# Kernel optimization log

Hardware: AMD Instinct MI355X
Metric: run time of the kernel (lower is better)

Reference implementation:

```python
import jax, jax.numpy as jnp
import numpy as np

B, S, H = 4, 4096, 768
NB = 16            # n_blocks (first factor)
BSZ = H // NB      # 48, block size
LN_EPS = 1e-12


def setup_inputs() -> dict:
    key = jax.random.key(0)
    ks = jax.random.split(key, 6)
    hidden_states = jax.random.normal(ks[0], (B, S, H), dtype=jnp.float32)
    # Monarch factors: B1 has NB blocks of (BSZ,BSZ); B2 has BSZ blocks of (NB,NB)
    w1_blocks = jax.random.normal(ks[1], (NB, BSZ, BSZ), dtype=jnp.float32) / np.sqrt(BSZ)
    w2_blocks = jax.random.normal(ks[2], (BSZ, NB, NB), dtype=jnp.float32) / np.sqrt(NB)
    gate_w = jax.random.normal(ks[3], (H, H), dtype=jnp.float32) / np.sqrt(H)
    gate_b = jnp.zeros((H,), dtype=jnp.float32)
    out_w = jax.random.normal(ks[4], (H, H), dtype=jnp.float32) / np.sqrt(H)
    out_b = jnp.zeros((H,), dtype=jnp.float32)
    ln_gamma = jnp.ones((H,), dtype=jnp.float32)
    ln_beta = jnp.zeros((H,), dtype=jnp.float32)
    return {
        "hidden_states": hidden_states,
        "w1_blocks": w1_blocks,
        "w2_blocks": w2_blocks,
        "gate_w": gate_w,
        "gate_b": gate_b,
        "out_w": out_w,
        "out_b": out_b,
        "ln_gamma": ln_gamma,
        "ln_beta": ln_beta,
    }


def _monarch(x, w1, w2):
    # x: [B, S, H]; Monarch product P B2 P B1 applied to last dim.
    b, s, h = x.shape
    y = x.reshape(b, s, NB, BSZ)
    y = jnp.einsum('bski,kij->bskj', y, w1)      # block-diag (NB blocks of BSZxBSZ)
    y = jnp.swapaxes(y, -1, -2)                  # permute: [B,S,BSZ,NB]
    y = jnp.einsum('bsqi,qij->bsqj', y, w2)      # block-diag (BSZ blocks of NBxNB)
    y = jnp.swapaxes(y, -1, -2)                  # permute back: [B,S,NB,BSZ]
    return y.reshape(b, s, h)


def _layernorm(x, gamma, beta, eps):
    mu = jnp.mean(x, axis=-1, keepdims=True)
    var = jnp.mean(jnp.square(x - mu), axis=-1, keepdims=True)
    return (x - mu) * jax.lax.rsqrt(var + eps) * gamma + beta


def reference(hidden_states, w1_blocks, w2_blocks, gate_w, gate_b,
              out_w, out_b, ln_gamma, ln_beta):
    residual = hidden_states
    mixed = _monarch(hidden_states, w1_blocks, w2_blocks)
    gate = jax.nn.sigmoid(hidden_states @ gate_w.T + gate_b)
    h = mixed * gate
    h = h @ out_w.T + out_b
    # dropout is identity in eval / p=0
    return _layernorm(h + residual, ln_gamma, ln_beta, LN_EPS)
```

## Files before the change

### kernel.cpp

```cpp
#include <hip/hip_runtime.h>
#include <hip/hip_bf16.h>
#include <stdint.h>

#define HD 768

typedef __attribute__((ext_vector_type(8))) short bf16x8;
typedef __attribute__((ext_vector_type(4))) float f32x4;
typedef __attribute__((ext_vector_type(4))) unsigned short u16x4;

typedef __attribute__((address_space(3))) void lds_void_t;
typedef const __attribute__((address_space(1))) void gbl_void_t;

__device__ inline void gload_lds16(const void* g, void* l) {
  __builtin_amdgcn_global_load_lds((gbl_void_t*)g, (lds_void_t*)l, 16, 0, 0);
}

__device__ inline unsigned short f2bf(float f) {
  union { float f; unsigned int u; } v; v.f = f;
  return (unsigned short)((v.u + 0x7fffu + ((v.u >> 16) & 1u)) >> 16);
}
__device__ inline float bf2f(unsigned short u) {
  union { unsigned int uu; float f; } v; v.uu = ((unsigned int)u) << 16;
  return v.f;
}

#define BAR() asm volatile("s_barrier" ::: "memory")
#define LGKM(N) { asm volatile("s_waitcnt lgkmcnt(" #N ")" ::: "memory"); __builtin_amdgcn_sched_barrier(0); }
#define VMC(N) asm volatile("s_waitcnt vmcnt(" #N ")" ::: "memory")

__global__ void prep_all_kernel(const float* __restrict__ x,
                                const float* __restrict__ gw, const float* __restrict__ ow,
                                const float* __restrict__ w1, const float* __restrict__ w2,
                                unsigned short* __restrict__ xb,
                                unsigned short* __restrict__ Gwb,
                                unsigned short* __restrict__ Opk,
                                unsigned short* __restrict__ w1f,
                                unsigned short* __restrict__ w2f) {
  int bid = blockIdx.x;
  if (bid < 12288) {
    int i = bid * 256 + threadIdx.x;
    float4 v = ((const float4*)x)[i];
    ushort4 o;
    o.x = f2bf(v.x); o.y = f2bf(v.y); o.z = f2bf(v.z); o.w = f2bf(v.w);
    ((ushort4*)xb)[i] = o;
  } else if (bid < 14592) {
    int e = (bid - 12288) * 256 + threadIdx.x;
    Gwb[e] = f2bf(gw[e]);
  } else if (bid < 14880) {
    int r = (bid - 14592) * 256 + threadIdx.x;
    int lane = r & 63;
    int ks = (r >> 6) % 24;
    int nt = r / (24 * 64);
    int n = nt * 16 + (lane & 15);
    int k = ks * 32 + (lane >> 4) * 8;
    bf16x8 pack;
#pragma unroll
    for (int j = 0; j < 8; ++j) pack[j] = (short)f2bf(ow[(size_t)n * HD + k + j]);
    *(bf16x8*)(Opk + (size_t)r * 8) = pack;
  } else if (bid < 14904) {
    int e = (bid - 14880) * 256 + threadIdx.x;
    int lane = e & 63, fi = e >> 6;
    int ks = fi & 1, nt = (fi >> 1) % 3, k = fi / 6;
    int lrr = lane & 15, lgg = lane >> 4;
    int q = nt * 16 + lrr;
    bf16x8 pack;
#pragma unroll
    for (int j = 0; j < 8; ++j) {
      int kk = ks * 32 + lgg * 8 + j;
      float v = (kk < 48) ? w1[(k * 48 + kk) * 48 + q] : 0.0f;
      pack[j] = (short)f2bf(v);
    }
    *(bf16x8*)(w1f + (size_t)e * 8) = pack;
  } else {
    int e = (bid - 14904) * 256 + threadIdx.x;
    int lane = e & 63, q = e >> 6;
    int lrr = lane & 15, lgg = lane >> 4;
    bf16x8 pack;
#pragma unroll
    for (int j = 0; j < 8; ++j) {
      int kk = lgg * 8 + j;
      float v = (kk < 16) ? w2[(q * 16 + kk) * 16 + lrr] : 0.0f;
      pack[j] = (short)f2bf(v);
    }
    *(bf16x8*)(w2f + (size_t)e * 8) = pack;
  }
}

__global__ __launch_bounds__(256, 2)
void monarch_kernel(const unsigned short* __restrict__ xb,
                    const unsigned short* __restrict__ w1f,
                    const unsigned short* __restrict__ w2f,
                    unsigned short* __restrict__ mx) {
  __shared__ __align__(16) unsigned char zl[49152];
  const int tid = threadIdx.x, lane = tid & 63, wid = tid >> 6;
  const int lr = lane & 15, lg = lane >> 4;
  const size_t m0 = (size_t)blockIdx.x * 32;

#pragma unroll
  for (int kb = 0; kb < 4; ++kb) {
    const int k = wid * 4 + kb;
    const unsigned short* wf = w1f + (size_t)(k * 6) * 512 + lane * 8;
    bf16x8 b00 = *(const bf16x8*)(wf + 0 * 512);
    bf16x8 b01 = *(const bf16x8*)(wf + 1 * 512);
    bf16x8 b10 = *(const bf16x8*)(wf + 2 * 512);
    bf16x8 b11 = *(const bf16x8*)(wf + 3 * 512);
    bf16x8 b20 = *(const bf16x8*)(wf + 4 * 512);
    bf16x8 b21 = *(const bf16x8*)(wf + 5 * 512);
#pragma unroll
    for (int mt = 0; mt < 2; ++mt) {
      const unsigned short* ar = xb + (m0 + mt * 16 + lr) * 768 + k * 48;
      bf16x8 a0 = *(const bf16x8*)(ar + lg * 8);
      bf16x8 a1 = (bf16x8){0, 0, 0, 0, 0, 0, 0, 0};
      if (lg < 2) a1 = *(const bf16x8*)(ar + 32 + lg * 8);
      f32x4 c0 = {0, 0, 0, 0}, c1 = {0, 0, 0, 0}, c2 = {0, 0, 0, 0};
      c0 = __builtin_amdgcn_mfma_f32_16x16x32_bf16(a0, b00, c0, 0, 0, 0);
      c0 = __builtin_amdgcn_mfma_f32_16x16x32_bf16(a1, b01, c0, 0, 0, 0);
      c1 = __builtin_amdgcn_mfma_f32_16x16x32_bf16(a0, b10, c1, 0, 0, 0);
      c1 = __builtin_amdgcn_mfma_f32_16x16x32_bf16(a1, b11, c1, 0, 0, 0);
      c2 = __builtin_amdgcn_mfma_f32_16x16x32_bf16(a0, b20, c2, 0, 0, 0);
      c2 = __builtin_amdgcn_mfma_f32_16x16x32_bf16(a1, b21, c2, 0, 0, 0);
#pragma unroll
      for (int i = 0; i < 4; ++i) {
        int row = mt * 16 + lg * 4 + i;
        int base = row * 1536 + k * 2;
        int swz = (row & 7) << 4;
        *(unsigned short*)(zl + ((base + (0 * 16 + lr) * 32) ^ swz)) = f2bf(c0[i]);
        *(unsigned short*)(zl + ((base + (1 * 16 + lr) * 32) ^ swz)) = f2bf(c1[i]);
        *(unsigned short*)(zl + ((base + (2 * 16 + lr) * 32) ^ swz)) = f2bf(c2[i]);
      }
    }
  }
  __syncthreads();

  unsigned int upk[2][4][6];
#pragma unroll
  for (int qq = 0; qq < 12; ++qq) {
    const int q = wid * 12 + qq;
    bf16x8 bw = *(const bf16x8*)(w2f + (size_t)q * 512 + lane * 8);
#pragma unroll
    for (int mt = 0; mt < 2; ++mt) {
      int row = mt * 16 + lr;
      int off = (row * 1536 + (lg < 2 ? q * 32 + lg * 16 : 0)) ^ ((row & 7) << 4);
      bf16x8 a = *(const bf16x8*)(zl + off);
      if (lg >= 2) a = (bf16x8){0, 0, 0, 0, 0, 0, 0, 0};
      f32x4 c = {0, 0, 0, 0};
      c = __builtin_amdgcn_mfma_f32_16x16x32_bf16(a, bw, c, 0, 0, 0);
#pragma unroll
      for (int i = 0; i < 4; ++i) {
        unsigned int h = (unsigned int)f2bf(c[i]);
        if (qq & 1) upk[mt][i][qq >> 1] |= (h << 16);
        else        upk[mt][i][qq >> 1] = h;
      }
    }
  }
  __syncthreads();

  const int wq0 = wid * 12;
#pragma unroll
  for (int mt = 0; mt < 2; ++mt) {
#pragma unroll
    for (int i = 0; i < 4; ++i) {
      int row = mt * 16 + lg * 4 + i;
      int base = row * 1536 + lr * 96 + wq0 * 2;
      int swz = (row & 7) << 4;
#pragma unroll
      for (int p = 0; p < 3; ++p) {
        uint2 v; v.x = upk[mt][i][p * 2]; v.y = upk[mt][i][p * 2 + 1];
        *(uint2*)(zl + ((base + p * 8) ^ swz)) = v;
      }
    }
  }
  __syncthreads();

#pragma unroll
  for (int p = 0; p < 12; ++p) {
    int id = p * 256 + tid;
    int row = id / 96, w16 = id % 96;
    int by = (row * 1536 + w16 * 16) ^ ((row & 7) << 4);
    f32x4 v = *(const f32x4*)(zl + by);
    *(f32x4*)((unsigned char*)mx + (m0 + row) * 1536 + w16 * 16) = v;
  }
}

__global__ __launch_bounds__(256, 2)
void gate_mix_kernel(const unsigned short* __restrict__ xb,
                     const unsigned short* __restrict__ Gwb,
                     const float* __restrict__ gate_b,
                     const unsigned short* __restrict__ mx,
                     unsigned short* __restrict__ hb) {
  __shared__ __align__(16) unsigned char lds[81920];
  const int tid = threadIdx.x, lane = tid & 63;
  const int wid = tid >> 6, wm = wid >> 1, wn = wid & 1;
  const int lr = lane & 15, lg = lane >> 4;

  const int b = blockIdx.x;
  const int work = (b & 7) * 64 + (b >> 3);
  const int panel = work >> 2, nwin = work & 3;
  const size_t m0 = (size_t)panel * 128;
  const int n0 = nwin * 192;

  const int r0 = tid >> 3;
  const int sw = ((tid & 7) << 4) ^ ((r0 & 7) << 4);
  const int o0 = (0 * 32 + r0) * 1536 + sw;
  const int o1 = (1 * 32 + r0) * 1536 + sw;
  const int o2 = (2 * 32 + r0) * 1536 + sw;
  const int o3 = (3 * 32 + r0) * 1536 + sw;
  const int o4 = (4 * 32 + r0) * 1536 + sw;
  const int o5 = (5 * 32 + r0) * 1536 + sw;
  const unsigned char* aS = (const unsigned char*)xb + m0 * 1536;
  const unsigned char* bS = (const unsigned char*)Gwb + (size_t)n0 * 1536;

#define STAGE_A(KT, BUF) { const unsigned char* sp = aS + (KT) * 128; \
    gload_lds16(sp + o0, lds + (BUF) * 16384 + tid * 16); \
    gload_lds16(sp + o1, lds + (BUF) * 16384 + 4096 + tid * 16); \
    gload_lds16(sp + o2, lds + (BUF) * 16384 + 8192 + tid * 16); \
    gload_lds16(sp + o3, lds + (BUF) * 16384 + 12288 + tid * 16); }
#define STAGE_B(KT, BUF) { const unsigned char* sp = bS + (KT) * 128; \
    gload_lds16(sp + o0, lds + 32768 + (BUF) * 24576 + tid * 16); \
    gload_lds16(sp + o1, lds + 32768 + (BUF) * 24576 + 4096 + tid * 16); \
    gload_lds16(sp + o2, lds + 32768 + (BUF) * 24576 + 8192 + tid * 16); \
    gload_lds16(sp + o3, lds + 32768 + (BUF) * 24576 + 12288 + tid * 16); \
    gload_lds16(sp + o4, lds + 32768 + (BUF) * 24576 + 16384 + tid * 16); \
    gload_lds16(sp + o5, lds + 32768 + (BUF) * 24576 + 20480 + tid * 16); }

  const int sx0 = (lg * 16) ^ ((lr & 7) << 4);
  const int sx1 = sx0 ^ 64;
  const unsigned char* baA0 = lds + (wm * 64 + lr) * 128 + sx0;
  const unsigned char* baA1 = lds + (wm * 64 + lr) * 128 + sx1;
  const unsigned char* baB0 = lds + 32768 + (wn * 96 + lr) * 128 + sx0;
  const unsigned char* baB1 = lds + 32768 + (wn * 96 + lr) * 128 + sx1;

  f32x4 acc[4][6];
#pragma unroll
  for (int mt = 0; mt < 4; ++mt)
#pragma unroll
    for (int nt = 0; nt < 6; ++nt) acc[mt][nt] = (f32x4){0, 0, 0, 0};

  bf16x8 aA[4], aB[4];
  bf16x8 bB0[6], bB1[6];

#define RD_AA(BUF) { _Pragma("unroll") for (int mt = 0; mt < 4; ++mt) \
      aA[mt] = *(const bf16x8*)(baA0 + (BUF) * 16384 + mt * 2048); }
#define RD_AB(BUF) { _Pragma("unroll") for (int mt = 0; mt < 4; ++mt) \
      aB[mt] = *(const bf16x8*)(baA1 + (BUF) * 16384 + mt * 2048); }
#define RD_B0(BUF) { _Pragma("unroll") for (int nt = 0; nt < 6; ++nt) \
      bB0[nt] = *(const bf16x8*)(baB0 + (BUF) * 24576 + nt * 2048); }
#define RD_B1(BUF) { _Pragma("unroll") for (int nt = 0; nt < 6; ++nt) \
      bB1[nt] = *(const bf16x8*)(baB1 + (BUF) * 24576 + nt * 2048); }
#define MM24(AR, BR) { __builtin_amdgcn_s_setprio(1); \
    _Pragma("unroll") for (int mt = 0; mt < 4; ++mt) \
    _Pragma("unroll") for (int nt = 0; nt < 6; ++nt) \
      acc[mt][nt] = __builtin_amdgcn_mfma_f32_16x16x32_bf16(AR[mt], BR[nt], acc[mt][nt], 0, 0, 0); \
    __builtin_amdgcn_s_setprio(0); }

#define KT_BODY(KT, BUF, STG, VN) { \
    RD_AB(BUF); RD_B1(BUF); \
    LGKM(10); MM24(aA, bB0); \
    LGKM(0); \
    BAR(); \
    if (STG) { STAGE_A((KT) + 2, BUF); STAGE_B((KT) + 2, BUF); } \
    VMC(VN); \
    BAR(); \
    RD_AA((BUF) ^ 1); RD_B0((BUF) ^ 1); \
    MM24(aB, bB1); }

  STAGE_A(0, 0); STAGE_B(0, 0); STAGE_A(1, 1); STAGE_B(1, 1);
  VMC(10);
  BAR();
  RD_AA(0); RD_B0(0);

#pragma unroll 1
  for (int kt = 0; kt < 10; kt += 2) {
    KT_BODY(kt, 0, 1, 10);
    KT_BODY(kt + 1, 1, 1, 10);
  }
  KT_BODY(10, 0, 0, 0);
  RD_AB(1); RD_B1(1);
  LGKM(10); MM24(aA, bB0);
  LGKM(0);  MM24(aB, bB1);

#pragma unroll
  for (int nt = 0; nt < 6; ++nt) {
    const int col = n0 + wn * 96 + nt * 16 + lr;
    const float gbv = gate_b[col];
#pragma unroll
    for (int mt = 0; mt < 4; ++mt) {
#pragma unroll
      for (int i = 0; i < 4; ++i) {
        size_t row = m0 + wm * 64 + mt * 16 + lg * 4 + i;
        float g = acc[mt][nt][i] + gbv;
        float s = 1.0f / (1.0f + __expf(-g));
        float mval = bf2f(mx[row * 768 + col]);
        hb[row * 768 + col] = f2bf(s * mval);
      }
    }
  }
#undef STAGE_A
#undef STAGE_B
#undef RD_AA
#undef RD_AB
#undef RD_B0
#undef RD_B1
#undef MM24
#undef KT_BODY
}

__global__ __launch_bounds__(512, 2)
void out_ln_kernel(const unsigned short* __restrict__ hb,
                   const unsigned short* __restrict__ Opk,
                   const float* __restrict__ out_b,
                   const unsigned short* __restrict__ xb,
                   const float* __restrict__ gamma,
                   const float* __restrict__ beta,
                   float* __restrict__ out) {
  __shared__ __align__(16) unsigned char lds[16384];
  __shared__ float psum[64][8];
  __shared__ float psq[64][8];

  const int tid = threadIdx.x, lane = tid & 63, wid = tid >> 6;
  const int lr = lane & 15, lg = lane >> 4;
  const size_t m0 = (size_t)blockIdx.x * 64;

  const int srow = tid >> 3;
  const unsigned char* aSrc = (const unsigned char*)hb + (m0 + srow) * 1536
                              + (((tid & 7) << 4) ^ ((srow & 7) << 4));
#define STAGE_A(KT, BUF) gload_lds16(aSrc + (KT) * 128, lds + (BUF) * 8192 + tid * 16)

  const unsigned short* bBase = Opk + ((size_t)(wid * 6) * 24 * 64 + lane) * 8;
#define LOAD_B(KT, BR) { _Pragma("unroll") for (int nt = 0; nt < 6; ++nt) { \
      BR[nt * 2 + 0] = *(const bf16x8*)(bBase + nt * 12288 + ((KT) * 2 + 0) * 512); \
      BR[nt * 2 + 1] = *(const bf16x8*)(bBase + nt * 12288 + ((KT) * 2 + 1) * 512); } }

  const int sx0 = (lg * 16) ^ ((lr & 7) << 4);
  const unsigned char* baA0 = lds + lr * 128 + sx0;
  const unsigned char* baA1 = lds + lr * 128 + (sx0 ^ 64);
#define RD_A(BUF) { _Pragma("unroll") for (int mt = 0; mt < 4; ++mt) { \
      aF0[mt] = *(const bf16x8*)(baA0 + (BUF) * 8192 + mt * 2048); \
      aF1[mt] = *(const bf16x8*)(baA1 + (BUF) * 8192 + mt * 2048); } }

#define MM48(BR) { __builtin_amdgcn_s_setprio(1); \
    _Pragma("unroll") for (int mt = 0; mt < 4; ++mt) \
    _Pragma("unroll") for (int nt = 0; nt < 6; ++nt) { \
      acc[mt][nt] = __builtin_amdgcn_mfma_f32_16x16x32_bf16(aF0[mt], BR[nt * 2 + 0], acc[mt][nt], 0, 0, 0); \
      acc[mt][nt] = __builtin_amdgcn_mfma_f32_16x16x32_bf16(aF1[mt], BR[nt * 2 + 1], acc[mt][nt], 0, 0, 0); } \
    __builtin_amdgcn_s_setprio(0); }

  f32x4 acc[4][6];
#pragma unroll
  for (int mt = 0; mt < 4; ++mt)
#pragma unroll
    for (int nt = 0; nt < 6; ++nt) acc[mt][nt] = (f32x4){0, 0, 0, 0};

  bf16x8 aF0[4], aF1[4];
  bf16x8 bP[12], bQ[12];

#define KT_BODY(KT, BUF, BCUR, BNXT, LAST) { \
    if (!(LAST)) { STAGE_A((KT) + 1, (BUF) ^ 1); LOAD_B((KT) + 1, BNXT); } \
    RD_A(BUF); \
    LGKM(0); \
    if (!(LAST)) { VMC(13); } else { VMC(0); } \
    MM48(BCUR); \
    if (!(LAST)) { VMC(12); BAR(); } }

  STAGE_A(0, 0);
  LOAD_B(0, bP);
  VMC(12);
  BAR();

#pragma unroll 1
  for (int kt = 0; kt < 10; kt += 2) {
    KT_BODY(kt, 0, bP, bQ, 0);
    KT_BODY(kt + 1, 1, bQ, bP, 0);
  }
  KT_BODY(10, 0, bP, bQ, 0);
  KT_BODY(11, 1, bQ, bP, 1);

#pragma unroll
  for (int nt = 0; nt < 6; ++nt) {
    const int col = wid * 96 + nt * 16 + lr;
    const float obv = out_b[col];
#pragma unroll
    for (int mt = 0; mt < 4; ++mt) {
#pragma unroll
      for (int i = 0; i < 4; ++i) {
        size_t row = m0 + mt * 16 + lg * 4 + i;
        acc[mt][nt][i] += obv + bf2f(xb[row * 768 + col]);
      }
    }
  }
#pragma unroll
  for (int mt = 0; mt < 4; ++mt) {
#pragma unroll
    for (int i = 0; i < 4; ++i) {
      float s = 0.f, q = 0.f;
#pragma unroll
      for (int nt = 0; nt < 6; ++nt) { float v = acc[mt][nt][i]; s += v; q += v * v; }
#pragma unroll
      for (int off = 8; off >= 1; off >>= 1) {
        s += __shfl_xor(s, off);
        q += __shfl_xor(q, off);
      }
      if (lr == 0) {
        int rl = mt * 16 + lg * 4 + i;
        psum[rl][wid] = s; psq[rl][wid] = q;
      }
    }
  }
  __syncthreads();
#pragma unroll
  for (int mt = 0; mt < 4; ++mt) {
#pragma unroll
    for (int i = 0; i < 4; ++i) {
      int rl = mt * 16 + lg * 4 + i;
      float s = 0.f, q = 0.f;
#pragma unroll
      for (int w = 0; w < 8; ++w) { s += psum[rl][w]; q += psq[rl][w]; }
      float mu = s * (1.0f / 768.0f);
      float var = q * (1.0f / 768.0f) - mu * mu;
      var = var < 0.f ? 0.f : var;
      float rstd = rsqrtf(var + 1e-12f);
      size_t grow = m0 + rl;
#pragma unroll
      for (int nt = 0; nt < 6; ++nt) {
        int col = wid * 96 + nt * 16 + lr;
        out[grow * 768 + col] = (acc[mt][nt][i] - mu) * rstd * gamma[col] + beta[col];
      }
    }
  }
#undef STAGE_A
#undef LOAD_B
#undef RD_A
#undef MM48
#undef KT_BODY
}

extern "C" void kernel_launch(void* const* d_in, const int* in_sizes, int n_in,
                              void* d_out, int out_size, void* d_ws, size_t ws_size,
                              hipStream_t stream) {
  const float* x   = (const float*)d_in[0];
  const float* w1  = (const float*)d_in[1];
  const float* w2  = (const float*)d_in[2];
  const float* gw  = (const float*)d_in[3];
  const float* gb  = (const float*)d_in[4];
  const float* ow  = (const float*)d_in[5];
  const float* ob  = (const float*)d_in[6];
  const float* gam = (const float*)d_in[7];
  const float* bet = (const float*)d_in[8];
  float* out = (float*)d_out;

  char* ws = (char*)d_ws;
  unsigned short* xb  = (unsigned short*)(ws);
  unsigned short* hb  = (unsigned short*)(ws + 25165824);
  unsigned short* Gwb = (unsigned short*)(ws + 50331648);
  unsigned short* Opk = (unsigned short*)(ws + 51511296);
  unsigned short* w1f = (unsigned short*)(ws + 52690944);
  unsigned short* w2f = (unsigned short*)(ws + 52789248);
  unsigned short* mx  = (unsigned short*)d_out;

  prep_all_kernel<<<14916, 256, 0, stream>>>(x, gw, ow, w1, w2, xb, Gwb, Opk, w1f, w2f);
  monarch_kernel<<<512, 256, 0, stream>>>(xb, w1f, w2f, mx);
  gate_mix_kernel<<<512, 256, 0, stream>>>(xb, Gwb, gb, mx, hb);
  out_ln_kernel<<<256, 512, 0, stream>>>(hb, Opk, ob, xb, gam, bet, out);
}
```

Baseline: 98.21 us.

## Fuse monarch transform into prep kernel and stage epilogue operands through LDS

Merges the x fp32→bf16 conversion with the Monarch block-diagonal transform in one kernel. Each block converts 16 rows, keeps them in LDS and computes the mixed output directly, so the separate monarch launch and the xb reread go away. Monarch weights are now packed into registers per block instead of precomputed, which repeats that small conversion in every block. In gate_mix and out_ln, the epilogue operands (mx and the residual xb) are prefetched into LDS with async global_load_lds during the last MFMA step instead of scattered 2-byte global loads. This adds a 96KB LDS buffer in out_ln that may reduce occupancy.

```diff
diff --git a/kernel.cpp b/kernel.cpp
--- a/kernel.cpp
+++ b/kernel.cpp
@@ -28,26 +28,137 @@
 #define LGKM(N) { asm volatile("s_waitcnt lgkmcnt(" #N ")" ::: "memory"); __builtin_amdgcn_sched_barrier(0); }
 #define VMC(N) asm volatile("s_waitcnt vmcnt(" #N ")" ::: "memory")
 
-__global__ void prep_all_kernel(const float* __restrict__ x,
-                                const float* __restrict__ gw, const float* __restrict__ ow,
-                                const float* __restrict__ w1, const float* __restrict__ w2,
-                                unsigned short* __restrict__ xb,
-                                unsigned short* __restrict__ Gwb,
-                                unsigned short* __restrict__ Opk,
-                                unsigned short* __restrict__ w1f,
-                                unsigned short* __restrict__ w2f) {
+__global__ __launch_bounds__(256, 2)
+void prep_monarch_all_kernel(const float* __restrict__ x,
+                             const float* __restrict__ gw, const float* __restrict__ ow,
+                             const float* __restrict__ w1, const float* __restrict__ w2,
+                             unsigned short* __restrict__ xb,
+                             unsigned short* __restrict__ Gwb,
+                             unsigned short* __restrict__ Opk,
+                             unsigned short* __restrict__ mx) {
+  __shared__ __align__(16) unsigned char xtile[24576];
+  __shared__ __align__(16) unsigned char zl[24576];
   int bid = blockIdx.x;
-  if (bid < 12288) {
-    int i = bid * 256 + threadIdx.x;
-    float4 v = ((const float4*)x)[i];
-    ushort4 o;
-    o.x = f2bf(v.x); o.y = f2bf(v.y); o.z = f2bf(v.z); o.w = f2bf(v.w);
-    ((ushort4*)xb)[i] = o;
-  } else if (bid < 14592) {
-    int e = (bid - 12288) * 256 + threadIdx.x;
+  if (bid < 1024) {
+    const int tid = threadIdx.x, lane = tid & 63, wid = tid >> 6;
+    const int lr = lane & 15, lg = lane >> 4;
+    const size_t m0 = (size_t)bid * 16;
+
+    bf16x8 w1r[4][3][2];
+#pragma unroll
+    for (int kb = 0; kb < 4; ++kb) {
+      const int k = wid * 4 + kb;
+#pragma unroll
+      for (int nt = 0; nt < 3; ++nt) {
+        const int q = nt * 16 + lr;
+#pragma unroll
+        for (int ks = 0; ks < 2; ++ks) {
+          bf16x8 p;
+#pragma unroll
+          for (int j = 0; j < 8; ++j) {
+            int kk = ks * 32 + lg * 8 + j;
+            float v = (kk < 48) ? w1[(k * 48 + kk) * 48 + q] : 0.0f;
+            p[j] = (short)f2bf(v);
+          }
+          w1r[kb][nt][ks] = p;
+        }
+      }
+    }
+    bf16x8 w2r[12];
+#pragma unroll
+    for (int qq = 0; qq < 12; ++qq) {
+      const int q = wid * 12 + qq;
+      bf16x8 p;
+#pragma unroll
+      for (int j = 0; j < 8; ++j) {
+        int kk = lg * 8 + j;
+        float v = (kk < 16) ? w2[(q * 16 + kk) * 16 + lr] : 0.0f;
+        p[j] = (short)f2bf(v);
+      }
+      w2r[qq] = p;
+    }
+
+    const float4* xsrc = (const float4*)x + (size_t)bid * 3072;
+    ushort4* xdst = (ushort4*)xb + (size_t)bid * 3072;
+#pragma unroll
+    for (int p = 0; p < 12; ++p) {
+      int id = p * 256 + tid;
+      float4 v = xsrc[id];
+      ushort4 o;
+      o.x = f2bf(v.x); o.y = f2bf(v.y); o.z = f2bf(v.z); o.w = f2bf(v.w);
+      xdst[id] = o;
+      int row = id / 192, c4 = id - row * 192;
+      uint2 u2;
+      u2.x = (unsigned int)o.x | ((unsigned int)o.y << 16);
+      u2.y = (unsigned int)o.z | ((unsigned int)o.w << 16);
+      *(uint2*)(xtile + ((row * 1536 + c4 * 8) ^ ((row & 7) << 4))) = u2;
+    }
+    __syncthreads();
+
+#pragma unroll
+    for (int kb = 0; kb < 4; ++kb) {
+      const int k = wid * 4 + kb;
+      const int abase = lr * 1536 + k * 96;
+      const int aswz = (lr & 7) << 4;
+      bf16x8 a0 = *(const bf16x8*)(xtile + ((abase + lg * 16) ^ aswz));
+      bf16x8 a1 = (bf16x8){0, 0, 0, 0, 0, 0, 0, 0};
+      if (lg < 2) a1 = *(const bf16x8*)(xtile + ((abase + 64 + lg * 16) ^ aswz));
+#pragma unroll
+      for (int nt = 0; nt < 3; ++nt) {
+        f32x4 c = {0, 0, 0, 0};
+        c = __builtin_amdgcn_mfma_f32_16x16x32_bf16(a0, w1r[kb][nt][0], c, 0, 0, 0);
+        c = __builtin_amdgcn_mfma_f32_16x16x32_bf16(a1, w1r[kb][nt][1], c, 0, 0, 0);
+#pragma unroll
+        for (int i = 0; i < 4; ++i) {
+          int row = lg * 4 + i;
+          *(unsigned short*)(zl + ((row * 1536 + nt * 512 + lr * 32 + k * 2) ^ ((row & 7) << 4))) = f2bf(c[i]);
+        }
+      }
+    }
+    __syncthreads();
+
+    unsigned int upk[4][6];
+#pragma unroll
+    for (int qq = 0; qq < 12; ++qq) {
+      const int q = wid * 12 + qq;
+      bf16x8 a = (bf16x8){0, 0, 0, 0, 0, 0, 0, 0};
+      if (lg < 2) a = *(const bf16x8*)(zl + ((lr * 1536 + q * 32 + lg * 16) ^ ((lr & 7) << 4)));
+      f32x4 c = {0, 0, 0, 0};
+      c = __builtin_amdgcn_mfma_f32_16x16x32_bf16(a, w2r[qq], c, 0, 0, 0);
+#pragma unroll
+      for (int i = 0; i < 4; ++i) {
+        unsigned int h = (unsigned int)f2bf(c[i]);
+        if (qq & 1) upk[i][qq >> 1] |= (h << 16);
+        else        upk[i][qq >> 1] = h;
+      }
+    }
+    __syncthreads();
+
+#pragma unroll
+    for (int i = 0; i < 4; ++i) {
+      int row = lg * 4 + i;
+      int base = row * 1536 + lr * 96 + wid * 24;
+      int swz = (row & 7) << 4;
+#pragma unroll
+      for (int p = 0; p < 3; ++p) {
+        uint2 v; v.x = upk[i][p * 2]; v.y = upk[i][p * 2 + 1];
+        *(uint2*)(zl + ((base + p * 8) ^ swz)) = v;
+      }
+    }
+    __syncthreads();
+
+#pragma unroll
+    for (int p = 0; p < 6; ++p) {
+      int id = p * 256 + tid;
+      int row = id / 96, c16 = id - row * 96;
+      f32x4 v = *(const f32x4*)(zl + ((row * 1536 + c16 * 16) ^ ((row & 7) << 4)));
+      *(f32x4*)((unsigned char*)mx + (m0 + row) * 1536 + c16 * 16) = v;
+    }
+  } else if (bid < 3328) {
+    int e = (bid - 1024) * 256 + threadIdx.x;
     Gwb[e] = f2bf(gw[e]);
-  } else if (bid < 14880) {
-    int r = (bid - 14592) * 256 + threadIdx.x;
+  } else {
+    int r = (bid - 3328) * 256 + threadIdx.x;
     int lane = r & 63;
     int ks = (r >> 6) % 24;
     int nt = r / (24 * 64);
@@ -57,128 +168,6 @@
 #pragma unroll
     for (int j = 0; j < 8; ++j) pack[j] = (short)f2bf(ow[(size_t)n * HD + k + j]);
     *(bf16x8*)(Opk + (size_t)r * 8) = pack;
-  } else if (bid < 14904) {
-    int e = (bid - 14880) * 256 + threadIdx.x;
-    int lane = e & 63, fi = e >> 6;
-    int ks = fi & 1, nt = (fi >> 1) % 3, k = fi / 6;
-    int lrr = lane & 15, lgg = lane >> 4;
-    int q = nt * 16 + lrr;
-    bf16x8 pack;
-#pragma unroll
-    for (int j = 0; j < 8; ++j) {
-      int kk = ks * 32 + lgg * 8 + j;
-      float v = (kk < 48) ? w1[(k * 48 + kk) * 48 + q] : 0.0f;
-      pack[j] = (short)f2bf(v);
-    }
-    *(bf16x8*)(w1f + (size_t)e * 8) = pack;
-  } else {
-    int e = (bid - 14904) * 256 + threadIdx.x;
-    int lane = e & 63, q = e >> 6;
-    int lrr = lane & 15, lgg = lane >> 4;
-    bf16x8 pack;
-#pragma unroll
-    for (int j = 0; j < 8; ++j) {
-      int kk = lgg * 8 + j;
-      float v = (kk < 16) ? w2[(q * 16 + kk) * 16 + lrr] : 0.0f;
-      pack[j] = (short)f2bf(v);
-    }
-    *(bf16x8*)(w2f + (size_t)e * 8) = pack;
-  }
-}
-
-__global__ __launch_bounds__(256, 2)
-void monarch_kernel(const unsigned short* __restrict__ xb,
-                    const unsigned short* __restrict__ w1f,
-                    const unsigned short* __restrict__ w2f,
-                    unsigned short* __restrict__ mx) {
-  __shared__ __align__(16) unsigned char zl[49152];
-  const int tid = threadIdx.x, lane = tid & 63, wid = tid >> 6;
-  const int lr = lane & 15, lg = lane >> 4;
-  const size_t m0 = (size_t)blockIdx.x * 32;
-
-#pragma unroll
-  for (int kb = 0; kb < 4; ++kb) {
-    const int k = wid * 4 + kb;
-    const unsigned short* wf = w1f + (size_t)(k * 6) * 512 + lane * 8;
-    bf16x8 b00 = *(const bf16x8*)(wf + 0 * 512);
-    bf16x8 b01 = *(const bf16x8*)(wf + 1 * 512);
-    bf16x8 b10 = *(const bf16x8*)(wf + 2 * 512);
-    bf16x8 b11 = *(const bf16x8*)(wf + 3 * 512);
-    bf16x8 b20 = *(const bf16x8*)(wf + 4 * 512);
-    bf16x8 b21 = *(const bf16x8*)(wf + 5 * 512);
-#pragma unroll
-    for (int mt = 0; mt < 2; ++mt) {
-      const unsigned short* ar = xb + (m0 + mt * 16 + lr) * 768 + k * 48;
-      bf16x8 a0 = *(const bf16x8*)(ar + lg * 8);
-      bf16x8 a1 = (bf16x8){0, 0, 0, 0, 0, 0, 0, 0};
-      if (lg < 2) a1 = *(const bf16x8*)(ar + 32 + lg * 8);
-      f32x4 c0 = {0, 0, 0, 0}, c1 = {0, 0, 0, 0}, c2 = {0, 0, 0, 0};
-      c0 = __builtin_amdgcn_mfma_f32_16x16x32_bf16(a0, b00, c0, 0, 0, 0);
-      c0 = __builtin_amdgcn_mfma_f32_16x16x32_bf16(a1, b01, c0, 0, 0, 0);
-      c1 = __builtin_amdgcn_mfma_f32_16x16x32_bf16(a0, b10, c1, 0, 0, 0);
-      c1 = __builtin_amdgcn_mfma_f32_16x16x32_bf16(a1, b11, c1, 0, 0, 0);
-      c2 = __builtin_amdgcn_mfma_f32_16x16x32_bf16(a0, b20, c2, 0, 0, 0);
-      c2 = __builtin_amdgcn_mfma_f32_16x16x32_bf16(a1, b21, c2, 0, 0, 0);
-#pragma unroll
-      for (int i = 0; i < 4; ++i) {
-        int row = mt * 16 + lg * 4 + i;
-        int base = row * 1536 + k * 2;
-        int swz = (row & 7) << 4;
-        *(unsigned short*)(zl + ((base + (0 * 16 + lr) * 32) ^ swz)) = f2bf(c0[i]);
-        *(unsigned short*)(zl + ((base + (1 * 16 + lr) * 32) ^ swz)) = f2bf(c1[i]);
-        *(unsigned short*)(zl + ((base + (2 * 16 + lr) * 32) ^ swz)) = f2bf(c2[i]);
-      }
-    }
-  }
-  __syncthreads();
-
-  unsigned int upk[2][4][6];
-#pragma unroll
-  for (int qq = 0; qq < 12; ++qq) {
-    const int q = wid * 12 + qq;
-    bf16x8 bw = *(const bf16x8*)(w2f + (size_t)q * 512 + lane * 8);
-#pragma unroll
-    for (int mt = 0; mt < 2; ++mt) {
-      int row = mt * 16 + lr;
-      int off = (row * 1536 + (lg < 2 ? q * 32 + lg * 16 : 0)) ^ ((row & 7) << 4);
-      bf16x8 a = *(const bf16x8*)(zl + off);
-      if (lg >= 2) a = (bf16x8){0, 0, 0, 0, 0, 0, 0, 0};
-      f32x4 c = {0, 0, 0, 0};
-      c = __builtin_amdgcn_mfma_f32_16x16x32_bf16(a, bw, c, 0, 0, 0);
-#pragma unroll
-      for (int i = 0; i < 4; ++i) {
-        unsigned int h = (unsigned int)f2bf(c[i]);
-        if (qq & 1) upk[mt][i][qq >> 1] |= (h << 16);
-        else        upk[mt][i][qq >> 1] = h;
-      }
-    }
-  }
-  __syncthreads();
-
-  const int wq0 = wid * 12;
-#pragma unroll
-  for (int mt = 0; mt < 2; ++mt) {
-#pragma unroll
-    for (int i = 0; i < 4; ++i) {
-      int row = mt * 16 + lg * 4 + i;
-      int base = row * 1536 + lr * 96 + wq0 * 2;
-      int swz = (row & 7) << 4;
-#pragma unroll
-      for (int p = 0; p < 3; ++p) {
-        uint2 v; v.x = upk[mt][i][p * 2]; v.y = upk[mt][i][p * 2 + 1];
-        *(uint2*)(zl + ((base + p * 8) ^ swz)) = v;
-      }
-    }
-  }
-  __syncthreads();
-
-#pragma unroll
-  for (int p = 0; p < 12; ++p) {
-    int id = p * 256 + tid;
-    int row = id / 96, w16 = id % 96;
-    int by = (row * 1536 + w16 * 16) ^ ((row & 7) << 4);
-    f32x4 v = *(const f32x4*)(zl + by);
-    *(f32x4*)((unsigned char*)mx + (m0 + row) * 1536 + w16 * 16) = v;
   }
 }
 
@@ -276,21 +265,36 @@
   }
   KT_BODY(10, 0, 0, 0);
   RD_AB(1); RD_B1(1);
-  LGKM(10); MM24(aA, bB0);
-  LGKM(0);  MM24(aB, bB1);
+  LGKM(0);
+  BAR();
+  {
+    const unsigned char* ms = (const unsigned char*)mx + m0 * 1536 + (size_t)n0 * 2;
+#pragma unroll
+    for (int p = 0; p < 12; ++p) {
+      int id = p * 256 + tid;
+      int row = id / 24, c16 = id - row * 24;
+      gload_lds16(ms + row * 1536 + c16 * 16, lds + id * 16);
+    }
+  }
+  MM24(aA, bB0);
+  MM24(aB, bB1);
+  VMC(0);
+  BAR();
 
 #pragma unroll
   for (int nt = 0; nt < 6; ++nt) {
     const int col = n0 + wn * 96 + nt * 16 + lr;
+    const int cl = wn * 96 + nt * 16 + lr;
     const float gbv = gate_b[col];
 #pragma unroll
     for (int mt = 0; mt < 4; ++mt) {
 #pragma unroll
       for (int i = 0; i < 4; ++i) {
-        size_t row = m0 + wm * 64 + mt * 16 + lg * 4 + i;
+        int rl = wm * 64 + mt * 16 + lg * 4 + i;
+        size_t row = m0 + rl;
         float g = acc[mt][nt][i] + gbv;
         float s = 1.0f / (1.0f + __expf(-g));
-        float mval = bf2f(mx[row * 768 + col]);
+        float mval = bf2f(*(const unsigned short*)(lds + rl * 384 + cl * 2));
         hb[row * 768 + col] = f2bf(s * mval);
       }
     }
@@ -314,6 +318,7 @@
                    const float* __restrict__ beta,
                    float* __restrict__ out) {
   __shared__ __align__(16) unsigned char lds[16384];
+  __shared__ __align__(16) unsigned char xlds[98304];
   __shared__ float psum[64][8];
   __shared__ float psq[64][8];
 
@@ -354,13 +359,13 @@
   bf16x8 aF0[4], aF1[4];
   bf16x8 bP[12], bQ[12];
 
-#define KT_BODY(KT, BUF, BCUR, BNXT, LAST) { \
-    if (!(LAST)) { STAGE_A((KT) + 1, (BUF) ^ 1); LOAD_B((KT) + 1, BNXT); } \
+#define KT_BODY(KT, BUF, BCUR, BNXT) { \
+    STAGE_A((KT) + 1, (BUF) ^ 1); LOAD_B((KT) + 1, BNXT); \
     RD_A(BUF); \
     LGKM(0); \
-    if (!(LAST)) { VMC(13); } else { VMC(0); } \
+    VMC(13); \
     MM48(BCUR); \
-    if (!(LAST)) { VMC(12); BAR(); } }
+    VMC(12); BAR(); }
 
   STAGE_A(0, 0);
   LOAD_B(0, bP);
@@ -369,11 +374,25 @@
 
 #pragma unroll 1
   for (int kt = 0; kt < 10; kt += 2) {
-    KT_BODY(kt, 0, bP, bQ, 0);
-    KT_BODY(kt + 1, 1, bQ, bP, 0);
-  }
-  KT_BODY(10, 0, bP, bQ, 0);
-  KT_BODY(11, 1, bQ, bP, 1);
+    KT_BODY(kt, 0, bP, bQ);
+    KT_BODY(kt + 1, 1, bQ, bP);
+  }
+  KT_BODY(10, 0, bP, bQ);
+  {
+    const unsigned char* xs = (const unsigned char*)xb + m0 * 1536;
+#pragma unroll
+    for (int p = 0; p < 12; ++p) {
+      int id = p * 512 + tid;
+      int row = id / 96, c16 = id - row * 96;
+      gload_lds16(xs + row * 1536 + c16 * 16, xlds + id * 16);
+    }
+  }
+  RD_A(1);
+  LGKM(0);
+  VMC(12);
+  MM48(bQ);
+  VMC(0);
+  BAR();
 
 #pragma unroll
   for (int nt = 0; nt < 6; ++nt) {
@@ -383,8 +402,8 @@
     for (int mt = 0; mt < 4; ++mt) {
 #pragma unroll
       for (int i = 0; i < 4; ++i) {
-        size_t row = m0 + mt * 16 + lg * 4 + i;
-        acc[mt][nt][i] += obv + bf2f(xb[row * 768 + col]);
+        int rl = mt * 16 + lg * 4 + i;
+        acc[mt][nt][i] += obv + bf2f(*(const unsigned short*)(xlds + rl * 1536 + col * 2));
       }
     }
   }
@@ -453,12 +472,9 @@
   unsigned short* hb  = (unsigned short*)(ws + 25165824);
   unsigned short* Gwb = (unsigned short*)(ws + 50331648);
   unsigned short* Opk = (unsigned short*)(ws + 51511296);
-  unsigned short* w1f = (unsigned short*)(ws + 52690944);
-  unsigned short* w2f = (unsigned short*)(ws + 52789248);
   unsigned short* mx  = (unsigned short*)d_out;
 
-  prep_all_kernel<<<14916, 256, 0, stream>>>(x, gw, ow, w1, w2, xb, Gwb, Opk, w1f, w2f);
-  monarch_kernel<<<512, 256, 0, stream>>>(xb, w1f, w2f, mx);
+  prep_monarch_all_kernel<<<3616, 256, 0, stream>>>(x, gw, ow, w1, w2, xb, Gwb, Opk, mx);
   gate_mix_kernel<<<512, 256, 0, stream>>>(xb, Gwb, gb, mx, hb);
   out_ln_kernel<<<256, 512, 0, stream>>>(hb, Opk, ob, xb, gam, bet, out);
 }
```

Result: slower. 151.2 us (+53.9%).
